# Kernel tuning notes

Measured on AMD Instinct MI355X. Metric: run time of the kernel, lower is better.

Reference implementation:

```python
import jax, jax.numpy as jnp
import numpy as np

ALPHA = 1.0

def setup_inputs() -> dict:
    key = jax.random.key(0)
    X = jax.random.normal(key, (2048, 128), dtype=jnp.float32)
    return {"X": X}

def reference(X) -> jnp.ndarray:
    # pairwise squared L2 distances, same math as ((X[None]-X[:,None])**2).sum(-1)
    diff = X[None, :, :] - X[:, None, :]          # [N, N, F]
    d2 = jnp.sum(diff * diff, axis=-1)            # [N, N]
    # track_running_stats=True, sigma=None -> sigma^2 = alpha * mean(d2) (detached)
    sigma_square = ALPHA * jax.lax.stop_gradient(jnp.mean(d2))
    return jnp.exp(-d2 / (2.0 * sigma_square))
```

## Files before the change

kernel.cpp:

```cpp
#include <hip/hip_runtime.h>
#include <stdint.h>

#define N 2048
#define F 128
#define ALPHA 1.0f
#define PREP_BLOCKS 128

typedef __bf16 bf16x8 __attribute__((ext_vector_type(8)));
typedef float f32x4 __attribute__((ext_vector_type(4)));

static constexpr size_t WS_XS  = 0;
static constexpr size_t WS_N   = (size_t)N * F * 2;
static constexpr size_t WS_SF  = WS_N + (size_t)N * 4;
static constexpr size_t WS_NSF = WS_SF + (size_t)F * 4;
static constexpr size_t WS_ZERO_BYTES = (size_t)F * 4 + 4;

__global__ __launch_bounds__(256) void gk_prep(const float* __restrict__ X,
                                               ushort* __restrict__ Xs,
                                               float* __restrict__ nrm,
                                               float* __restrict__ s_final,
                                               float* __restrict__ nsum_final) {
    __shared__ float s_lds[F];
    __shared__ float nw_lds[4];
    const int t = threadIdx.x;
    if (t < F) s_lds[t] = 0.f;
    __syncthreads();

    const int r    = t >> 4;
    const int kidx = t & 15;
    const int k0   = kidx * 8;
    const int row  = blockIdx.x * 16 + r;

    const float4* px = reinterpret_cast<const float4*>(X + (size_t)row * F + k0);
    float4 v0 = px[0], v1 = px[1];
    float xv[8] = {v0.x, v0.y, v0.z, v0.w, v1.x, v1.y, v1.z, v1.w};

    uint32_t us[8];
    float xb[8];
    float ns = 0.f;
#pragma unroll
    for (int j = 0; j < 8; ++j) {
        uint32_t u = __float_as_uint(xv[j]);
        u = (u + 0x7FFFu + ((u >> 16) & 1u)) >> 16;
        us[j] = u;
        float fb = __uint_as_float(u << 16);
        xb[j] = fb;
        ns += fb * fb;
    }
    uint4 packed;
    packed.x = us[0] | (us[1] << 16);
    packed.y = us[2] | (us[3] << 16);
    packed.z = us[4] | (us[5] << 16);
    packed.w = us[6] | (us[7] << 16);
    *reinterpret_cast<uint4*>(Xs + (size_t)blockIdx.x * 2048 + kidx * 128 + r * 8) = packed;

    float nsr = ns;
#pragma unroll
    for (int off = 1; off < 16; off <<= 1) nsr += __shfl_xor(nsr, off, 64);
    if (kidx == 0) nrm[row] = nsr;
#pragma unroll
    for (int off = 16; off < 64; off <<= 1) nsr += __shfl_xor(nsr, off, 64);
    if ((t & 63) == 0) nw_lds[t >> 6] = nsr;

#pragma unroll
    for (int j = 0; j < 8; ++j) {
        float cj = xb[j];
        cj += __shfl_xor(cj, 16, 64);
        cj += __shfl_xor(cj, 32, 64);
        if ((t & 48) == 0) atomicAdd(&s_lds[k0 + j], cj);
    }
    __syncthreads();

    if (t < F) atomicAdd(&s_final[t], s_lds[t]);
    if (t == 0) atomicAdd(nsum_final, nw_lds[0] + nw_lds[1] + nw_lds[2] + nw_lds[3]);
}

__global__ __launch_bounds__(256) void gk_main(const __bf16* __restrict__ Xs,
                                               const float* __restrict__ nrm,
                                               const float* __restrict__ s_final,
                                               const float* __restrict__ nsum_final,
                                               float* __restrict__ out) {
    const int t = threadIdx.x;
    const int wave = t >> 6, lane = t & 63;
    const int quad = lane >> 4, l16 = lane & 15;

    const int row0 = blockIdx.y * 128 + wave * 32;
    const int col0 = blockIdx.x * 64;

    bf16x8 afr[2][4], bfr[4][4];
#pragma unroll
    for (int mi = 0; mi < 2; ++mi) {
        const size_t gbase = (size_t)((row0 + mi * 16) >> 4) * 2048;
#pragma unroll
        for (int kc = 0; kc < 4; ++kc)
            afr[mi][kc] = *reinterpret_cast<const bf16x8*>(
                Xs + gbase + (kc * 4 + quad) * 128 + l16 * 8);
    }
#pragma unroll
    for (int ni = 0; ni < 4; ++ni) {
        const size_t gbase = (size_t)((col0 + ni * 16) >> 4) * 2048;
#pragma unroll
        for (int kc = 0; kc < 4; ++kc)
            bfr[ni][kc] = *reinterpret_cast<const bf16x8*>(
                Xs + gbase + (kc * 4 + quad) * 128 + l16 * 8);
    }

    float nr[2];
#pragma unroll
    for (int mi = 0; mi < 2; ++mi) nr[mi] = nrm[row0 + mi * 16 + l16];
    f32x4 ncv[4];
#pragma unroll
    for (int ni = 0; ni < 4; ++ni)
        ncv[ni] = *reinterpret_cast<const f32x4*>(nrm + col0 + ni * 16 + quad * 4);

    float c0 = s_final[2 * lane], c1 = s_final[2 * lane + 1];
    float nsum = *nsum_final;
    float v = c0 * c0 + c1 * c1;
#pragma unroll
    for (int off = 32; off; off >>= 1) v += __shfl_xor(v, off, 64);
    const float invn = 1.f / (float)N;
    const float meand2 = 2.f * invn * (nsum - v * invn);
    const float scale = -1.f / (2.f * ALPHA * meand2);

#pragma unroll
    for (int mi = 0; mi < 2; ++mi) {
        float* orow = out + (size_t)(row0 + mi * 16 + l16) * N + col0 + quad * 4;
#pragma unroll
        for (int ni = 0; ni < 4; ++ni) {
            f32x4 acc = {0.f, 0.f, 0.f, 0.f};
#pragma unroll
            for (int kc = 0; kc < 4; ++kc)
                acc = __builtin_amdgcn_mfma_f32_16x16x32_bf16(bfr[ni][kc], afr[mi][kc], acc, 0, 0, 0);
            f32x4 rv;
#pragma unroll
            for (int rg = 0; rg < 4; ++rg) {
                float d2 = fmaxf(nr[mi] + ncv[ni][rg] - 2.f * acc[rg], 0.f);
                rv[rg] = __expf(scale * d2);
            }
            __builtin_nontemporal_store(rv, reinterpret_cast<f32x4*>(orow + ni * 16));
        }
    }
}

extern "C" void kernel_launch(void* const* d_in, const int* in_sizes, int n_in,
                              void* d_out, int out_size, void* d_ws, size_t ws_size,
                              hipStream_t stream) {
    const float* X = (const float*)d_in[0];
    float* out = (float*)d_out;
    char* ws = (char*)d_ws;

    ushort* Xs         = (ushort*)(ws + WS_XS);
    float*  nrm        = (float*)(ws + WS_N);
    float*  s_final    = (float*)(ws + WS_SF);
    float*  nsum_final = (float*)(ws + WS_NSF);

    hipMemsetAsync(ws + WS_SF, 0, WS_ZERO_BYTES, stream);
    gk_prep<<<PREP_BLOCKS, 256, 0, stream>>>(X, Xs, nrm, s_final, nsum_final);

    dim3 grid(N / 64, N / 128);
    gk_main<<<grid, 256, 0, stream>>>((const __bf16*)Xs, nrm, s_final, nsum_final, out);
}
```

Baseline: 69.91 us.

## Replace global atomics and memset with per-block partials reduced in main kernel

The prep kernel now writes per-block column sums and norm sums to partial buffers instead of atomically accumulating into zeroed globals, which removes the hipMemsetAsync launch and the cross-block atomics. Each main-kernel block re-reduces the 128x128 partials (64KB read per block, served mostly from cache) plus an LDS reduction and a block barrier. The exp is also switched to a native exp2 with the log2(e) factor folded into the scale. The trade is one fewer launch and no atomics against redundant reduction work and an extra sync in every main block.

```diff
diff --git a/kernel.cpp b/kernel.cpp
--- a/kernel.cpp
+++ b/kernel.cpp
@@ -9,17 +9,16 @@
 typedef __bf16 bf16x8 __attribute__((ext_vector_type(8)));
 typedef float f32x4 __attribute__((ext_vector_type(4)));
 
-static constexpr size_t WS_XS  = 0;
-static constexpr size_t WS_N   = (size_t)N * F * 2;
-static constexpr size_t WS_SF  = WS_N + (size_t)N * 4;
-static constexpr size_t WS_NSF = WS_SF + (size_t)F * 4;
-static constexpr size_t WS_ZERO_BYTES = (size_t)F * 4 + 4;
+static constexpr size_t WS_XS    = 0;
+static constexpr size_t WS_N     = (size_t)N * F * 2;
+static constexpr size_t WS_SP    = WS_N + (size_t)N * 4;
+static constexpr size_t WS_NSUMP = WS_SP + (size_t)F * PREP_BLOCKS * 4;
 
 __global__ __launch_bounds__(256) void gk_prep(const float* __restrict__ X,
                                                ushort* __restrict__ Xs,
                                                float* __restrict__ nrm,
-                                               float* __restrict__ s_final,
-                                               float* __restrict__ nsum_final) {
+                                               float* __restrict__ s_part,
+                                               float* __restrict__ nsum_part) {
     __shared__ float s_lds[F];
     __shared__ float nw_lds[4];
     const int t = threadIdx.x;
@@ -71,15 +70,16 @@
     }
     __syncthreads();
 
-    if (t < F) atomicAdd(&s_final[t], s_lds[t]);
-    if (t == 0) atomicAdd(nsum_final, nw_lds[0] + nw_lds[1] + nw_lds[2] + nw_lds[3]);
+    if (t < F) s_part[(size_t)t * PREP_BLOCKS + blockIdx.x] = s_lds[t];
+    if (t == 0) nsum_part[blockIdx.x] = nw_lds[0] + nw_lds[1] + nw_lds[2] + nw_lds[3];
 }
 
 __global__ __launch_bounds__(256) void gk_main(const __bf16* __restrict__ Xs,
                                                const float* __restrict__ nrm,
-                                               const float* __restrict__ s_final,
-                                               const float* __restrict__ nsum_final,
+                                               const float* __restrict__ s_part,
+                                               const float* __restrict__ nsum_part,
                                                float* __restrict__ out) {
+    __shared__ float red[8];
     const int t = threadIdx.x;
     const int wave = t >> 6, lane = t & 63;
     const int quad = lane >> 4, l16 = lane & 15;
@@ -113,14 +113,27 @@
     for (int ni = 0; ni < 4; ++ni)
         ncv[ni] = *reinterpret_cast<const f32x4*>(nrm + col0 + ni * 16 + quad * 4);
 
-    float c0 = s_final[2 * lane], c1 = s_final[2 * lane + 1];
-    float nsum = *nsum_final;
-    float v = c0 * c0 + c1 * c1;
+    const f32x4* sp = reinterpret_cast<const f32x4*>(
+        s_part + (size_t)(t >> 1) * PREP_BLOCKS + (t & 1) * 64);
+    f32x4 pa = {0.f, 0.f, 0.f, 0.f};
 #pragma unroll
-    for (int off = 32; off; off >>= 1) v += __shfl_xor(v, off, 64);
+    for (int q = 0; q < 16; ++q) pa += sp[q];
+    float sh_half = pa[0] + pa[1] + pa[2] + pa[3];
+    float Sk = sh_half + __shfl_xor(sh_half, 1, 64);
+    float vv = (t & 1) ? 0.f : Sk * Sk;
+    float nsv = (t < PREP_BLOCKS) ? nsum_part[t] : 0.f;
+#pragma unroll
+    for (int off = 32; off; off >>= 1) {
+        vv  += __shfl_xor(vv, off, 64);
+        nsv += __shfl_xor(nsv, off, 64);
+    }
+    if (lane == 0) { red[wave * 2] = vv; red[wave * 2 + 1] = nsv; }
+    __syncthreads();
+    const float V  = red[0] + red[2] + red[4] + red[6];
+    const float NS = red[1] + red[3] + red[5] + red[7];
     const float invn = 1.f / (float)N;
-    const float meand2 = 2.f * invn * (nsum - v * invn);
-    const float scale = -1.f / (2.f * ALPHA * meand2);
+    const float meand2 = 2.f * invn * (NS - V * invn);
+    const float scale2 = -1.44269504088896f / (2.f * ALPHA * meand2);
 
 #pragma unroll
     for (int mi = 0; mi < 2; ++mi) {
@@ -135,7 +148,7 @@
 #pragma unroll
             for (int rg = 0; rg < 4; ++rg) {
                 float d2 = fmaxf(nr[mi] + ncv[ni][rg] - 2.f * acc[rg], 0.f);
-                rv[rg] = __expf(scale * d2);
+                rv[rg] = __builtin_amdgcn_exp2f(scale2 * d2);
             }
             __builtin_nontemporal_store(rv, reinterpret_cast<f32x4*>(orow + ni * 16));
         }
@@ -149,14 +162,13 @@
     float* out = (float*)d_out;
     char* ws = (char*)d_ws;
 
-    ushort* Xs         = (ushort*)(ws + WS_XS);
-    float*  nrm        = (float*)(ws + WS_N);
-    float*  s_final    = (float*)(ws + WS_SF);
-    float*  nsum_final = (float*)(ws + WS_NSF);
+    ushort* Xs      = (ushort*)(ws + WS_XS);
+    float*  nrm     = (float*)(ws + WS_N);
+    float*  s_part  = (float*)(ws + WS_SP);
+    float*  nsum_p  = (float*)(ws + WS_NSUMP);
 
-    hipMemsetAsync(ws + WS_SF, 0, WS_ZERO_BYTES, stream);
-    gk_prep<<<PREP_BLOCKS, 256, 0, stream>>>(X, Xs, nrm, s_final, nsum_final);
+    gk_prep<<<PREP_BLOCKS, 256, 0, stream>>>(X, Xs, nrm, s_part, nsum_p);
 
     dim3 grid(N / 64, N / 128);
-    gk_main<<<grid, 256, 0, stream>>>((const __bf16*)Xs, nrm, s_final, nsum_final, out);
+    gk_main<<<grid, 256, 0, stream>>>((const __bf16*)Xs, nrm, s_part, nsum_p, out);
 }
```

Measured after the change: 66.59 us. 1.05x faster.
